# Optimization experiments

Measured on AMD Instinct MI355X. Metric: run time of the kernel, lower is better.

Reference implementation:

```python
import jax, jax.numpy as jnp
from jax import lax
import numpy as np

B, C, T = 128, 64, 750
NOUT, K, HID = 4, 16, 128


def _conv(x, w, b=None):
    y = lax.conv_general_dilated(x, w, (1, 1), 'VALID', dimension_numbers=('NCHW', 'OIHW', 'NCHW'))
    return y if b is None else y + b[None, :, None, None]


def _bn(x, g, b, m, v):
    s = g / jnp.sqrt(v + 1e-5)
    return (x - m[None, :, None, None]) * s[None, :, None, None] + b[None, :, None, None]


def _pool(x):
    return lax.reduce_window(x, -jnp.inf, lax.max, (1, 1, 3, 1), (1, 1, 3, 1), 'VALID')


def _backbone(x, ct_w, ct_b, cs_w, bn1, c2_w, bn2, c3_w, bn3, c4_w, bn4, fc_w, fc_b):
    # x: (B, C, T) -> (B, 1, T, C)  (braindecode transpose_time_to_spat)
    h = jnp.transpose(x, (0, 2, 1))[:, None]
    h = _conv(h, ct_w, ct_b)              # (B,25,T-9,C)
    h = _conv(h, cs_w)                    # (B,25,T-9,1)
    h = _pool(jax.nn.elu(_bn(h, *bn1)))   # (B,25,247,1)
    h = _pool(jax.nn.elu(_bn(_conv(h, c2_w), *bn2)))  # (B,50,79,1)
    h = _pool(jax.nn.elu(_bn(_conv(h, c3_w), *bn3)))  # (B,100,23,1)
    h = _pool(jax.nn.elu(_bn(_conv(h, c4_w), *bn4)))  # (B,200,4,1)
    h = _conv(h, fc_w, fc_b)              # (B,NOUT,1,1)
    return h[:, :, 0, 0]                  # (B,NOUT)


def _heads(feats, cluster_ids, hW1, hb1, hW2, hb2):
    # gather per-sample head params, batched small GEMMs (MoE-style dispatch)
    h = jax.nn.relu(jnp.einsum('bf,bfh->bh', feats, hW1[cluster_ids]) + hb1[cluster_ids])
    return jnp.einsum('bh,bho->bo', h, hW2[cluster_ids]) + hb2[cluster_ids]


def setup_inputs() -> dict:
    key = jax.random.key(0)
    ks = jax.random.split(key, 40)
    n = lambda i, shape, s=0.1: jax.random.normal(ks[i], shape, dtype=jnp.float32) * s
    u = lambda i, shape: jax.random.uniform(ks[i], shape, dtype=jnp.float32) + 0.5
    inp = {
        'x': n(0, (B, C, T), 1.0),
        'cluster_ids': jax.random.randint(ks[1], (B,), 0, K),
        'ct_w': n(2, (25, 1, 10, 1)), 'ct_b': n(3, (25,)),
        'cs_w': n(4, (25, 25, 1, C)),
        'bn1_g': u(5, (25,)), 'bn1_b': n(6, (25,)), 'bn1_m': n(7, (25,)), 'bn1_v': u(8, (25,)),
        'c2_w': n(9, (50, 25, 10, 1)),
        'bn2_g': u(10, (50,)), 'bn2_b': n(11, (50,)), 'bn2_m': n(12, (50,)), 'bn2_v': u(13, (50,)),
        'c3_w': n(14, (100, 50, 10, 1)),
        'bn3_g': u(15, (100,)), 'bn3_b': n(16, (100,)), 'bn3_m': n(17, (100,)), 'bn3_v': u(18, (100,)),
        'c4_w': n(19, (200, 100, 10, 1)),
        'bn4_g': u(20, (200,)), 'bn4_b': n(21, (200,)), 'bn4_m': n(22, (200,)), 'bn4_v': u(23, (200,)),
        'fc_w': n(24, (NOUT, 200, 4, 1)), 'fc_b': n(25, (NOUT,)),
        'hW1': n(26, (K, NOUT, HID)), 'hb1': n(27, (K, HID)),
        'hW2': n(28, (K, HID, NOUT)), 'hb2': n(29, (K, NOUT)),
    }
    return inp


def reference(x, cluster_ids, ct_w, ct_b, cs_w,
              bn1_g, bn1_b, bn1_m, bn1_v, c2_w,
              bn2_g, bn2_b, bn2_m, bn2_v, c3_w,
              bn3_g, bn3_b, bn3_m, bn3_v, c4_w,
              bn4_g, bn4_b, bn4_m, bn4_v, fc_w, fc_b,
              hW1, hb1, hW2, hb2):
    feats = _backbone(x, ct_w, ct_b, cs_w,
                      (bn1_g, bn1_b, bn1_m, bn1_v), c2_w,
                      (bn2_g, bn2_b, bn2_m, bn2_v), c3_w,
                      (bn3_g, bn3_b, bn3_m, bn3_v), c4_w,
                      (bn4_g, bn4_b, bn4_m, bn4_v), fc_w, fc_b)
    return _heads(feats, cluster_ids, hW1, hb1, hW2, hb2)
```

## Files before the change

kernel.cpp:

```cpp
#include <hip/hip_runtime.h>
#include <hip/hip_bf16.h>
#include <math.h>

typedef __attribute__((ext_vector_type(8))) short short8v;
typedef __attribute__((ext_vector_type(4))) float f32x4;

#define F_S1 0
#define F_H1 32
#define F_S2 64
#define F_H2 128
#define F_S3 192
#define F_H3 320
#define F_S4 448
#define F_H4 704
#define F_B1 960
#define F_P4 1024
#define F_END (1024 + 128*200*4)
#define H_BASE (F_END * 2)
#define H_P1  H_BASE
#define H_P2  (H_P1 + 128*25*248)
#define H_P3  (H_P2 + 128*50*80)
#define H_WA1 (H_P3 + 128*100*24)
#define H_WA2 (H_WA1 + 32*640)
#define H_WA3 (H_WA2 + 64*320)
#define H_WA4 (H_WA3 + 112*640)

__device__ __forceinline__ float eluf(float v) {
    return v > 0.f ? v : (expf(v) - 1.f);
}
__device__ __forceinline__ float ldf(const float* p) { return *p; }
__device__ __forceinline__ float ldf(const __hip_bfloat16* p) { return __bfloat162float(*p); }
__device__ __forceinline__ void stf(float* p, float v) { *p = v; }
__device__ __forceinline__ void stf(__hip_bfloat16* p, float v) { *p = __float2bfloat16(v); }

__device__ __forceinline__ void ld4(const float* p, float* v) {
    float2 a = *(const float2*)p, c = *(const float2*)(p + 2);
    v[0] = a.x; v[1] = a.y; v[2] = c.x; v[3] = c.y;
}
__device__ __forceinline__ void ld4(const __hip_bfloat16* p, float* v) {
    uint2 u = *(const uint2*)p;
    v[0] = __uint_as_float((u.x & 0xffffu) << 16);
    v[1] = __uint_as_float(u.x & 0xffff0000u);
    v[2] = __uint_as_float((u.y & 0xffffu) << 16);
    v[3] = __uint_as_float(u.y & 0xffff0000u);
}

#define N_WA1 (32*640)
#define N_WA2 (64*320)
#define N_WA3 (112*640)
#define N_WA4 (208*1280)
#define N_WTOT (N_WA1 + N_WA2 + N_WA3 + N_WA4)

__global__ __launch_bounds__(256) void k_pre2(
    const float* __restrict__ ct_w, const float* __restrict__ ct_b,
    const float* __restrict__ cs_w,
    const float* __restrict__ g1, const float* __restrict__ b1,
    const float* __restrict__ m1, const float* __restrict__ v1,
    const float* __restrict__ w2,
    const float* __restrict__ g2, const float* __restrict__ b2,
    const float* __restrict__ m2, const float* __restrict__ v2,
    const float* __restrict__ w3,
    const float* __restrict__ g3, const float* __restrict__ b3,
    const float* __restrict__ m3, const float* __restrict__ v3,
    const float* __restrict__ w4,
    const float* __restrict__ g4, const float* __restrict__ b4,
    const float* __restrict__ m4, const float* __restrict__ v4,
    float* __restrict__ ws) {
    __hip_bfloat16* wsh = (__hip_bfloat16*)ws;
    int t = blockIdx.x * 256 + threadIdx.x;
    if (t < N_WA1) {
        int o = t / 640, kv = t - o * 640, kk = kv / 64, c = kv - kk * 64;
        float s = 0.f;
        if (o < 25)
            for (int i = 0; i < 25; ++i)
                s += cs_w[(o * 25 + i) * 64 + c] * ct_w[i * 10 + kk];
        wsh[H_WA1 + t] = __float2bfloat16(s);
    } else if (t < N_WA1 + N_WA2) {
        int u = t - N_WA1;
        int o = u / 320, kv = u - o * 320, kk = kv / 32, c = kv - kk * 32;
        float s = (o < 50 && c < 25) ? w2[(o * 25 + c) * 10 + kk] : 0.f;
        wsh[H_WA2 + u] = __float2bfloat16(s);
    } else if (t < N_WA1 + N_WA2 + N_WA3) {
        int u = t - N_WA1 - N_WA2;
        int o = u / 640, kv = u - o * 640, kk = kv / 64, c = kv - kk * 64;
        float s = (o < 100 && c < 50) ? w3[(o * 50 + c) * 10 + kk] : 0.f;
        wsh[H_WA3 + u] = __float2bfloat16(s);
    } else if (t < N_WTOT) {
        int u = t - N_WA1 - N_WA2 - N_WA3;
        int o = u / 1280, kv = u - o * 1280, kk = kv / 128, c = kv - kk * 128;
        float s = (o < 200 && c < 100) ? w4[(o * 100 + c) * 10 + kk] : 0.f;
        wsh[H_WA4 + u] = __float2bfloat16(s);
    } else {
        int j = t - N_WTOT;
        if (j < 25) {
            float sc = g1[j] / sqrtf(v1[j] + 1e-5f);
            ws[F_S1 + j] = sc; ws[F_H1 + j] = b1[j] - m1[j] * sc;
        } else if (j >= 32 && j < 82) {
            int ch = j - 32;
            float sc = g2[ch] / sqrtf(v2[ch] + 1e-5f);
            ws[F_S2 + ch] = sc; ws[F_H2 + ch] = b2[ch] - m2[ch] * sc;
        } else if (j >= 96 && j < 196) {
            int ch = j - 96;
            float sc = g3[ch] / sqrtf(v3[ch] + 1e-5f);
            ws[F_S3 + ch] = sc; ws[F_H3 + ch] = b3[ch] - m3[ch] * sc;
        } else if (j >= 224 && j < 424) {
            int ch = j - 224;
            float sc = g4[ch] / sqrtf(v4[ch] + 1e-5f);
            ws[F_S4 + ch] = sc; ws[F_H4 + ch] = b4[ch] - m4[ch] * sc;
        } else if (j >= 448 && j < 473) {
            int o = j - 448;
            float s = 0.f;
            for (int i = 0; i < 25; ++i) {
                float cs = 0.f;
                for (int c = 0; c < 64; ++c) cs += cs_w[(o * 25 + i) * 64 + c];
                s += cs * ct_b[i];
            }
            ws[F_B1 + o] = s;
        }
    }
}

template<typename IT, typename OT, int CIN, int CINP, int COUT,
         int TINLEN, int TSIN, int TPOOL, int TSOUT,
         int PT, int OSPLIT, int NCT, int CSPLIT, int ROWS, bool BIAS>
__global__ __launch_bounds__(256) void k_convmf(
    const IT* __restrict__ in, OT* __restrict__ outp,
    const __hip_bfloat16* __restrict__ Wa,
    const float* __restrict__ sv, const float* __restrict__ hv,
    const float* __restrict__ bv) {
    constexpr int K    = CINP * 10;
    constexpr int NS   = K / 32;
    constexpr int CB   = CINP / 32;
    constexpr int NOT  = (COUT + 15) / 16;
    constexpr int NOTP = (NOT + OSPLIT - 1) / OSPLIT;
    constexpr int SWM  = (CINP >= 64) ? 7 : 3;
    constexpr int EBS  = NCT * 16;
    constexpr int CTW  = NCT / CSPLIT;
    constexpr int CHR  = ROWS / 4;

    int bx = blockIdx.x, b = blockIdx.y;
    int tt = bx / OSPLIT, os = bx % OSPLIT;
    int p0 = tt * PT;
    int PTb = min(PT, TPOOL - p0);
    int t0 = 3 * p0;
    int otLo = os * NOTP;
    int NOTb = min(NOT - otLo, NOTP);

    __shared__ __hip_bfloat16 xb[ROWS * CINP];
    __shared__ float eb[NOTP * 16 * EBS];

    for (int f = threadIdx.x; f < CIN * CHR; f += 256) {
        int c = f / CHR, j = f - c * CHR;
        int t = t0 + 4 * j;
        const IT* src = in + ((size_t)b * CIN + c) * TSIN + t;
        float v[4];
        if (t + 3 < TINLEN) {
            ld4(src, v);
        } else {
#pragma unroll
            for (int e = 0; e < 4; ++e)
                v[e] = (t + e < TINLEN) ? ldf(src + e) : 0.f;
        }
#pragma unroll
        for (int e = 0; e < 4; ++e) {
            int r = 4 * j + e;
            xb[r * CINP + (c ^ (8 * (r & SWM)))] = __float2bfloat16(v[e]);
        }
    }
    if constexpr (CINP > CIN) {
        for (int f = threadIdx.x; f < (CINP - CIN) * ROWS; f += 256) {
            int c = CIN + f / ROWS, r = f % ROWS;
            xb[r * CINP + (c ^ (8 * (r & SWM)))] = __float2bfloat16(0.f);
        }
    }
    __syncthreads();

    int lane = threadIdx.x & 63, wid = threadIdx.x >> 6;
    int lo = lane & 15, kg = lane >> 4;
    int ctg = wid % CSPLIT;
    for (int oi = wid / CSPLIT; oi < NOTb; oi += 4 / CSPLIT) {
        int ot = otLo + oi;
        const short8v* Ap = (const short8v*)(Wa + (size_t)(ot * 16 + lo) * K);
        f32x4 acc[CTW];
#pragma unroll
        for (int q = 0; q < CTW; ++q) acc[q] = (f32x4){0.f, 0.f, 0.f, 0.f};
#pragma unroll
        for (int s = 0; s < NS; ++s) {
            short8v afr = Ap[s * 4 + kg];
            int kk = s / CB, cb = s - kk * CB;
#pragma unroll
            for (int q = 0; q < CTW; ++q) {
                int ct = ctg * CTW + q;
                int r = ct * 16 + lo + kk;
                int cs = (cb * 32 + kg * 8) ^ (8 * (r & SWM));
                short8v bfr = *(const short8v*)&xb[r * CINP + cs];
                acc[q] = __builtin_amdgcn_mfma_f32_16x16x32_bf16(afr, bfr, acc[q], 0, 0, 0);
            }
        }
#pragma unroll
        for (int q = 0; q < CTW; ++q) {
            int tloc = (ctg * CTW + q) * 16 + lo;
#pragma unroll
            for (int e = 0; e < 4; ++e) {
                int o2 = ot * 16 + kg * 4 + e;
                if (o2 < COUT) {
                    float a = acc[q][e];
                    if (BIAS) a += bv[o2];
                    eb[(o2 - otLo * 16) * EBS + tloc] = eluf(a * sv[o2] + hv[o2]);
                }
            }
        }
    }
    __syncthreads();

    int oLo = otLo * 16;
    int nO = min(COUT, (otLo + NOTb) * 16) - oLo;
    for (int i = threadIdx.x; i < nO * PT; i += 256) {
        int o = oLo + i / PT, pl = i % PT;
        if (pl < PTb) {
            const float* ep = eb + (o - oLo) * EBS + 3 * pl;
            float m = fmaxf(fmaxf(ep[0], ep[1]), ep[2]);
            stf(outp + ((size_t)b * COUT + o) * TSOUT + p0 + pl, m);
        }
    }
}

__global__ __launch_bounds__(128) void k_heads(
    const float* __restrict__ p4,
    const float* __restrict__ fcw, const float* __restrict__ fcb,
    const int* __restrict__ cids,
    const float* __restrict__ hW1, const float* __restrict__ hb1,
    const float* __restrict__ hW2, const float* __restrict__ hb2,
    float* __restrict__ out) {
    __shared__ float red[4][128];
    __shared__ float fs[4];
    int b = blockIdx.x, j = threadIdx.x;

    float pa[4] = {0.f, 0.f, 0.f, 0.f};
    for (int c = j; c < 200; c += 128) {
        const float* pp = p4 + ((size_t)b * 200 + c) * 4;
        float v0 = pp[0], v1 = pp[1], v2 = pp[2], v3 = pp[3];
#pragma unroll
        for (int o = 0; o < 4; ++o) {
            const float* fw = fcw + (o * 200 + c) * 4;
            pa[o] += fw[0] * v0 + fw[1] * v1 + fw[2] * v2 + fw[3] * v3;
        }
    }
#pragma unroll
    for (int o = 0; o < 4; ++o) red[o][j] = pa[o];
    __syncthreads();
    for (int s = 64; s > 0; s >>= 1) {
        if (j < s) {
#pragma unroll
            for (int o = 0; o < 4; ++o) red[o][j] += red[o][j + s];
        }
        __syncthreads();
    }
    if (j < 4) fs[j] = red[j][0] + fcb[j];
    __syncthreads();

    int cid = cids[b];
    float hvv = hb1[cid * 128 + j];
#pragma unroll
    for (int f = 0; f < 4; ++f) hvv += fs[f] * hW1[(cid * 4 + f) * 128 + j];
    hvv = fmaxf(hvv, 0.f);
#pragma unroll
    for (int o = 0; o < 4; ++o) red[o][j] = hvv * hW2[(cid * 128 + j) * 4 + o];
    __syncthreads();
    for (int s = 64; s > 0; s >>= 1) {
        if (j < s) {
#pragma unroll
            for (int o = 0; o < 4; ++o) red[o][j] += red[o][j + s];
        }
        __syncthreads();
    }
    if (j < 4) out[b * 4 + j] = red[j][0] + hb2[cid * 4 + j];
}

extern "C" void kernel_launch(void* const* d_in, const int* in_sizes, int n_in,
                              void* d_out, int out_size, void* d_ws, size_t ws_size,
                              hipStream_t stream) {
    (void)in_sizes; (void)n_in; (void)out_size; (void)ws_size;
    const float* x    = (const float*)d_in[0];
    const int*   cid  = (const int*)d_in[1];
    const float* ctw  = (const float*)d_in[2];
    const float* ctb  = (const float*)d_in[3];
    const float* csw  = (const float*)d_in[4];
    const float* g1 = (const float*)d_in[5],  *b1 = (const float*)d_in[6];
    const float* m1 = (const float*)d_in[7],  *v1 = (const float*)d_in[8];
    const float* w2 = (const float*)d_in[9];
    const float* g2 = (const float*)d_in[10], *b2 = (const float*)d_in[11];
    const float* m2 = (const float*)d_in[12], *v2 = (const float*)d_in[13];
    const float* w3 = (const float*)d_in[14];
    const float* g3 = (const float*)d_in[15], *b3 = (const float*)d_in[16];
    const float* m3 = (const float*)d_in[17], *v3 = (const float*)d_in[18];
    const float* w4 = (const float*)d_in[19];
    const float* g4 = (const float*)d_in[20], *b4 = (const float*)d_in[21];
    const float* m4 = (const float*)d_in[22], *v4 = (const float*)d_in[23];
    const float* fcw = (const float*)d_in[24], *fcb = (const float*)d_in[25];
    const float* hW1 = (const float*)d_in[26], *hb1 = (const float*)d_in[27];
    const float* hW2 = (const float*)d_in[28], *hb2 = (const float*)d_in[29];
    float* ws  = (float*)d_ws;
    __hip_bfloat16* wsh = (__hip_bfloat16*)d_ws;
    float* out = (float*)d_out;

    k_pre2<<<dim3((N_WTOT + 512 + 255) / 256), dim3(256), 0, stream>>>(
        ctw, ctb, csw, g1, b1, m1, v1, w2, g2, b2, m2, v2,
        w3, g3, b3, m3, v3, w4, g4, b4, m4, v4, ws);

    k_convmf<float, __hip_bfloat16, 64, 64, 25, 750, 750, 247, 248,
             32, 1, 6, 2, 112, true>
        <<<dim3(8, 128), dim3(256), 0, stream>>>(
            x, wsh + H_P1, wsh + H_WA1, ws + F_S1, ws + F_H1, ws + F_B1);
    k_convmf<__hip_bfloat16, __hip_bfloat16, 25, 32, 50, 247, 248, 79, 80,
             20, 1, 4, 1, 80, false>
        <<<dim3(4, 128), dim3(256), 0, stream>>>(
            wsh + H_P1, wsh + H_P2, wsh + H_WA2, ws + F_S2, ws + F_H2, ws + F_B1);
    k_convmf<__hip_bfloat16, __hip_bfloat16, 50, 64, 100, 79, 80, 23, 24,
             12, 2, 3, 1, 64, false>
        <<<dim3(4, 128), dim3(256), 0, stream>>>(
            wsh + H_P2, wsh + H_P3, wsh + H_WA3, ws + F_S3, ws + F_H3, ws + F_B1);
    k_convmf<__hip_bfloat16, float, 100, 128, 200, 23, 24, 4, 4,
             4, 4, 1, 1, 32, false>
        <<<dim3(4, 128), dim3(256), 0, stream>>>(
            wsh + H_P3, ws + F_P4, wsh + H_WA4, ws + F_S4, ws + F_H4, ws + F_B1);

    k_heads<<<dim3(128), dim3(128), 0, stream>>>(ws + F_P4, fcw, fcb, cid,
                                                 hW1, hb1, hW2, hb2, out);
}
```

Before: 94.57 us.

## Fuse conv2-4 and heads into one per-sample kernel with LDS-resident activations

Collapses the four templated conv launches plus the heads kernel into two kernels. A specialized first-layer conv writes a time-major, swizzled bf16 pooled output. A single 512-thread per-sample tail kernel then runs layers 2-4, pooling, the FC and the heads entirely in shared memory. This removes three launches and the global round trips of the intermediate activations. In exchange it uses only 128 blocks for the tail, so occupancy and parallelism drop, and the layer-4 output now passes through bf16 before the FC.

```diff
diff --git a/kernel.cpp b/kernel.cpp
--- a/kernel.cpp
+++ b/kernel.cpp
@@ -14,42 +14,29 @@
 #define F_S4 448
 #define F_H4 704
 #define F_B1 960
-#define F_P4 1024
-#define F_END (1024 + 128*200*4)
-#define H_BASE (F_END * 2)
+#define F_END 1024
+#define H_BASE (F_END*2)
 #define H_P1  H_BASE
-#define H_P2  (H_P1 + 128*25*248)
-#define H_P3  (H_P2 + 128*50*80)
-#define H_WA1 (H_P3 + 128*100*24)
+#define H_WA1 (H_P1 + 128*8192)
 #define H_WA2 (H_WA1 + 32*640)
 #define H_WA3 (H_WA2 + 64*320)
 #define H_WA4 (H_WA3 + 112*640)
-
-__device__ __forceinline__ float eluf(float v) {
-    return v > 0.f ? v : (expf(v) - 1.f);
-}
-__device__ __forceinline__ float ldf(const float* p) { return *p; }
-__device__ __forceinline__ float ldf(const __hip_bfloat16* p) { return __bfloat162float(*p); }
-__device__ __forceinline__ void stf(float* p, float v) { *p = v; }
-__device__ __forceinline__ void stf(__hip_bfloat16* p, float v) { *p = __float2bfloat16(v); }
-
-__device__ __forceinline__ void ld4(const float* p, float* v) {
-    float2 a = *(const float2*)p, c = *(const float2*)(p + 2);
-    v[0] = a.x; v[1] = a.y; v[2] = c.x; v[3] = c.y;
-}
-__device__ __forceinline__ void ld4(const __hip_bfloat16* p, float* v) {
-    uint2 u = *(const uint2*)p;
-    v[0] = __uint_as_float((u.x & 0xffffu) << 16);
-    v[1] = __uint_as_float(u.x & 0xffff0000u);
-    v[2] = __uint_as_float((u.y & 0xffffu) << 16);
-    v[3] = __uint_as_float(u.y & 0xffff0000u);
-}
 
 #define N_WA1 (32*640)
 #define N_WA2 (64*320)
 #define N_WA3 (112*640)
 #define N_WA4 (208*1280)
 #define N_WTOT (N_WA1 + N_WA2 + N_WA3 + N_WA4)
+
+__device__ __forceinline__ float eluf(float v) {
+    return v > 0.f ? v : (expf(v) - 1.f);
+}
+__device__ __forceinline__ float ldh(const __hip_bfloat16* p) { return __bfloat162float(*p); }
+
+__device__ __forceinline__ void ld4f(const float* p, float* v) {
+    float2 a = *(const float2*)p, c = *(const float2*)(p + 2);
+    v[0] = a.x; v[1] = a.y; v[2] = c.x; v[3] = c.y;
+}
 
 __global__ __launch_bounds__(256) void k_pre2(
     const float* __restrict__ ct_w, const float* __restrict__ ct_b,
@@ -120,134 +107,239 @@
     }
 }
 
-template<typename IT, typename OT, int CIN, int CINP, int COUT,
-         int TINLEN, int TSIN, int TPOOL, int TSOUT,
-         int PT, int OSPLIT, int NCT, int CSPLIT, int ROWS, bool BIAS>
-__global__ __launch_bounds__(256) void k_convmf(
-    const IT* __restrict__ in, OT* __restrict__ outp,
-    const __hip_bfloat16* __restrict__ Wa,
-    const float* __restrict__ sv, const float* __restrict__ hv,
-    const float* __restrict__ bv) {
-    constexpr int K    = CINP * 10;
-    constexpr int NS   = K / 32;
-    constexpr int CB   = CINP / 32;
-    constexpr int NOT  = (COUT + 15) / 16;
-    constexpr int NOTP = (NOT + OSPLIT - 1) / OSPLIT;
-    constexpr int SWM  = (CINP >= 64) ? 7 : 3;
-    constexpr int EBS  = NCT * 16;
-    constexpr int CTW  = NCT / CSPLIT;
-    constexpr int CHR  = ROWS / 4;
-
+template<int NS, int CB, int CINP>
+__device__ __forceinline__ f32x4 conv_item(
+    const __hip_bfloat16* __restrict__ Wrow,
+    const __hip_bfloat16* xb, int lo, int kg, int rowBase) {
+    constexpr int SWM = (CINP >= 64) ? 7 : 3;
+    const short8v* Ap = (const short8v*)Wrow;
+    f32x4 acc = {0.f, 0.f, 0.f, 0.f};
+#pragma unroll 1
+    for (int sb = 0; sb < NS; sb += 10) {
+        short8v af[10];
+#pragma unroll
+        for (int u = 0; u < 10; ++u) af[u] = Ap[(sb + u) * 4 + kg];
+#pragma unroll
+        for (int u = 0; u < 10; ++u) {
+            int s = sb + u;
+            int kk = s / CB, cb = s % CB;
+            int r = rowBase + lo + kk;
+            int cs = (cb * 32 + kg * 8) ^ (8 * (r & SWM));
+            short8v bf = *(const short8v*)&xb[r * CINP + cs];
+            acc = __builtin_amdgcn_mfma_f32_16x16x32_bf16(af[u], bf, acc, 0, 0, 0);
+        }
+    }
+    return acc;
+}
+
+__global__ __launch_bounds__(256) void k_conv1(
+    const float* __restrict__ x, float* __restrict__ ws) {
+    __hip_bfloat16* wsh = (__hip_bfloat16*)ws;
+    const __hip_bfloat16* Wa = wsh + H_WA1;
     int bx = blockIdx.x, b = blockIdx.y;
-    int tt = bx / OSPLIT, os = bx % OSPLIT;
-    int p0 = tt * PT;
-    int PTb = min(PT, TPOOL - p0);
-    int t0 = 3 * p0;
-    int otLo = os * NOTP;
-    int NOTb = min(NOT - otLo, NOTP);
-
-    __shared__ __hip_bfloat16 xb[ROWS * CINP];
-    __shared__ float eb[NOTP * 16 * EBS];
-
-    for (int f = threadIdx.x; f < CIN * CHR; f += 256) {
-        int c = f / CHR, j = f - c * CHR;
+    int tp0 = bx * 42;
+    int PTb = min(42, 247 - tp0);
+    int t0 = 126 * bx;
+
+    __shared__ __align__(16) __hip_bfloat16 xb[144 * 64];
+    __shared__ __align__(16) __hip_bfloat16 eb[32 * 128];
+
+    for (int f = threadIdx.x; f < 64 * 36; f += 256) {
+        int c = f / 36, j = f - c * 36;
         int t = t0 + 4 * j;
-        const IT* src = in + ((size_t)b * CIN + c) * TSIN + t;
+        const float* src = x + ((size_t)b * 64 + c) * 750 + t;
         float v[4];
-        if (t + 3 < TINLEN) {
-            ld4(src, v);
+        if (t + 3 < 750) {
+            ld4f(src, v);
         } else {
 #pragma unroll
-            for (int e = 0; e < 4; ++e)
-                v[e] = (t + e < TINLEN) ? ldf(src + e) : 0.f;
+            for (int e = 0; e < 4; ++e) v[e] = (t + e < 750) ? src[e] : 0.f;
         }
 #pragma unroll
         for (int e = 0; e < 4; ++e) {
             int r = 4 * j + e;
-            xb[r * CINP + (c ^ (8 * (r & SWM)))] = __float2bfloat16(v[e]);
-        }
-    }
-    if constexpr (CINP > CIN) {
-        for (int f = threadIdx.x; f < (CINP - CIN) * ROWS; f += 256) {
-            int c = CIN + f / ROWS, r = f % ROWS;
-            xb[r * CINP + (c ^ (8 * (r & SWM)))] = __float2bfloat16(0.f);
+            xb[r * 64 + (c ^ (8 * (r & 7)))] = __float2bfloat16(v[e]);
         }
     }
     __syncthreads();
 
     int lane = threadIdx.x & 63, wid = threadIdx.x >> 6;
     int lo = lane & 15, kg = lane >> 4;
-    int ctg = wid % CSPLIT;
-    for (int oi = wid / CSPLIT; oi < NOTb; oi += 4 / CSPLIT) {
-        int ot = otLo + oi;
-        const short8v* Ap = (const short8v*)(Wa + (size_t)(ot * 16 + lo) * K);
-        f32x4 acc[CTW];
-#pragma unroll
-        for (int q = 0; q < CTW; ++q) acc[q] = (f32x4){0.f, 0.f, 0.f, 0.f};
-#pragma unroll
-        for (int s = 0; s < NS; ++s) {
-            short8v afr = Ap[s * 4 + kg];
-            int kk = s / CB, cb = s - kk * CB;
-#pragma unroll
-            for (int q = 0; q < CTW; ++q) {
-                int ct = ctg * CTW + q;
-                int r = ct * 16 + lo + kk;
-                int cs = (cb * 32 + kg * 8) ^ (8 * (r & SWM));
-                short8v bfr = *(const short8v*)&xb[r * CINP + cs];
-                acc[q] = __builtin_amdgcn_mfma_f32_16x16x32_bf16(afr, bfr, acc[q], 0, 0, 0);
-            }
-        }
-#pragma unroll
-        for (int q = 0; q < CTW; ++q) {
-            int tloc = (ctg * CTW + q) * 16 + lo;
-#pragma unroll
-            for (int e = 0; e < 4; ++e) {
-                int o2 = ot * 16 + kg * 4 + e;
-                if (o2 < COUT) {
-                    float a = acc[q][e];
-                    if (BIAS) a += bv[o2];
-                    eb[(o2 - otLo * 16) * EBS + tloc] = eluf(a * sv[o2] + hv[o2]);
-                }
-            }
-        }
-    }
-    __syncthreads();
-
-    int oLo = otLo * 16;
-    int nO = min(COUT, (otLo + NOTb) * 16) - oLo;
-    for (int i = threadIdx.x; i < nO * PT; i += 256) {
-        int o = oLo + i / PT, pl = i % PT;
+    int ot = wid >> 1, ctg = wid & 1;
+    const short8v* Ap = (const short8v*)(Wa + (size_t)(ot * 16 + lo) * 640);
+    f32x4 acc[4];
+#pragma unroll
+    for (int q = 0; q < 4; ++q) acc[q] = (f32x4){0.f, 0.f, 0.f, 0.f};
+#pragma unroll 1
+    for (int sb = 0; sb < 20; sb += 10) {
+        short8v af[10];
+#pragma unroll
+        for (int u = 0; u < 10; ++u) af[u] = Ap[(sb + u) * 4 + kg];
+#pragma unroll
+        for (int u = 0; u < 10; ++u) {
+            int s = sb + u;
+            int kk = s >> 1, cb = s & 1;
+#pragma unroll
+            for (int q = 0; q < 4; ++q) {
+                int r = (ctg * 4 + q) * 16 + lo + kk;
+                int cs = (cb * 32 + kg * 8) ^ (8 * (r & 7));
+                short8v bf = *(const short8v*)&xb[r * 64 + cs];
+                acc[q] = __builtin_amdgcn_mfma_f32_16x16x32_bf16(af[u], bf, acc[q], 0, 0, 0);
+            }
+        }
+    }
+#pragma unroll
+    for (int q = 0; q < 4; ++q) {
+        int tloc = (ctg * 4 + q) * 16 + lo;
+#pragma unroll
+        for (int e = 0; e < 4; ++e) {
+            int o2 = ot * 16 + kg * 4 + e;
+            float a = acc[q][e] + ws[F_B1 + o2];
+            eb[o2 * 128 + tloc] = __float2bfloat16(eluf(a * ws[F_S1 + o2] + ws[F_H1 + o2]));
+        }
+    }
+    __syncthreads();
+
+    __hip_bfloat16* p1g = wsh + H_P1 + (size_t)b * 8192;
+    for (int i = threadIdx.x; i < 32 * 42; i += 256) {
+        int o = i / 42, pl = i - o * 42;
         if (pl < PTb) {
-            const float* ep = eb + (o - oLo) * EBS + 3 * pl;
-            float m = fmaxf(fmaxf(ep[0], ep[1]), ep[2]);
-            stf(outp + ((size_t)b * COUT + o) * TSOUT + p0 + pl, m);
-        }
-    }
-}
-
-__global__ __launch_bounds__(128) void k_heads(
-    const float* __restrict__ p4,
+            int tp = tp0 + pl;
+            float val = 0.f;
+            if (o < 25) {
+                const __hip_bfloat16* ep = eb + o * 128 + 3 * pl;
+                val = fmaxf(fmaxf(ldh(ep), ldh(ep + 1)), ldh(ep + 2));
+            }
+            p1g[tp * 32 + (o ^ (8 * (tp & 3)))] = __float2bfloat16(val);
+        }
+    }
+    if (bx == 5) {
+        for (int i = threadIdx.x; i < 9 * 32; i += 256) {
+            int r = 247 + i / 32, c = i & 31;
+            p1g[r * 32 + c] = __float2bfloat16(0.f);
+        }
+    }
+}
+
+__global__ __launch_bounds__(512) void k_tail(
+    const float* __restrict__ ws,
     const float* __restrict__ fcw, const float* __restrict__ fcb,
     const int* __restrict__ cids,
     const float* __restrict__ hW1, const float* __restrict__ hb1,
     const float* __restrict__ hW2, const float* __restrict__ hb2,
     float* __restrict__ out) {
+    const __hip_bfloat16* wsh = (const __hip_bfloat16*)ws;
+    const __hip_bfloat16* wa2 = wsh + H_WA2;
+    const __hip_bfloat16* wa3 = wsh + H_WA3;
+    const __hip_bfloat16* wa4 = wsh + H_WA4;
+    int b = blockIdx.x;
+    int tid = threadIdx.x;
+    int lane = tid & 63, wid = tid >> 6;
+    int lo = lane & 15, kg = lane >> 4;
+
+    __shared__ __align__(16) __hip_bfloat16 p1s[256 * 32];
+    __shared__ __align__(16) __hip_bfloat16 p2s[96 * 64];
+    __shared__ __align__(16) __hip_bfloat16 p3s[32 * 128];
+    __shared__ __align__(16) __hip_bfloat16 ebh[112 * 80];
+    __shared__ float p4s[200 * 4];
     __shared__ float red[4][128];
-    __shared__ float fs[4];
-    int b = blockIdx.x, j = threadIdx.x;
-
-    float pa[4] = {0.f, 0.f, 0.f, 0.f};
-    for (int c = j; c < 200; c += 128) {
-        const float* pp = p4 + ((size_t)b * 200 + c) * 4;
-        float v0 = pp[0], v1 = pp[1], v2 = pp[2], v3 = pp[3];
-#pragma unroll
-        for (int o = 0; o < 4; ++o) {
-            const float* fw = fcw + (o * 200 + c) * 4;
-            pa[o] += fw[0] * v0 + fw[1] * v1 + fw[2] * v2 + fw[3] * v3;
-        }
-    }
-#pragma unroll
-    for (int o = 0; o < 4; ++o) red[o][j] = pa[o];
+    __shared__ float fsf[4];
+
+    {
+        const uint4* src = (const uint4*)(wsh + H_P1 + (size_t)b * 8192);
+        uint4* dst = (uint4*)p1s;
+        dst[tid] = src[tid];
+        dst[tid + 512] = src[tid + 512];
+        uint4 z = {0, 0, 0, 0};
+        ((uint4*)p2s)[tid] = z;
+        if (tid < 256) ((uint4*)p2s)[512 + tid] = z;
+        ((uint4*)p3s)[tid] = z;
+    }
+    __syncthreads();
+
+    for (int c0 = 0; c0 < 4; ++c0) {
+        int tb = 60 * c0;
+        int PTb = (c0 == 3) ? 19 : 20;
+        for (int it = wid; it < 16; it += 8) {
+            int ot = it >> 2, ct = it & 3;
+            f32x4 a = conv_item<10, 1, 32>(wa2 + (size_t)(ot * 16 + lo) * 320,
+                                           p1s, lo, kg, tb + ct * 16);
+            int tloc = ct * 16 + lo;
+#pragma unroll
+            for (int e = 0; e < 4; ++e) {
+                int o2 = ot * 16 + kg * 4 + e;
+                ebh[o2 * 64 + tloc] =
+                    __float2bfloat16(eluf(a[e] * ws[F_S2 + o2] + ws[F_H2 + o2]));
+            }
+        }
+        __syncthreads();
+        for (int i = tid; i < 50 * 20; i += 512) {
+            int o = i / 20, pl = i - o * 20;
+            if (pl < PTb) {
+                int tp = 20 * c0 + pl;
+                const __hip_bfloat16* ep = ebh + o * 64 + 3 * pl;
+                float m = fmaxf(fmaxf(ldh(ep), ldh(ep + 1)), ldh(ep + 2));
+                p2s[tp * 64 + (o ^ (8 * (tp & 7)))] = __float2bfloat16(m);
+            }
+        }
+        __syncthreads();
+    }
+
+    for (int it = wid; it < 35; it += 8) {
+        int ot = it / 5, ct = it - 5 * ot;
+        f32x4 a = conv_item<20, 2, 64>(wa3 + (size_t)(ot * 16 + lo) * 640,
+                                       p2s, lo, kg, ct * 16);
+        int tloc = ct * 16 + lo;
+#pragma unroll
+        for (int e = 0; e < 4; ++e) {
+            int o2 = ot * 16 + kg * 4 + e;
+            ebh[o2 * 80 + tloc] =
+                __float2bfloat16(eluf(a[e] * ws[F_S3 + o2] + ws[F_H3 + o2]));
+        }
+    }
+    __syncthreads();
+    for (int i = tid; i < 100 * 23; i += 512) {
+        int o = i / 23, pl = i - 23 * o;
+        const __hip_bfloat16* ep = ebh + o * 80 + 3 * pl;
+        float m = fmaxf(fmaxf(ldh(ep), ldh(ep + 1)), ldh(ep + 2));
+        p3s[pl * 128 + (o ^ (8 * (pl & 7)))] = __float2bfloat16(m);
+    }
+    __syncthreads();
+
+    for (int it = wid; it < 13; it += 8) {
+        int ot = it;
+        f32x4 a = conv_item<40, 4, 128>(wa4 + (size_t)(ot * 16 + lo) * 1280,
+                                        p3s, lo, kg, 0);
+#pragma unroll
+        for (int e = 0; e < 4; ++e) {
+            int o2 = ot * 16 + kg * 4 + e;
+            ebh[o2 * 16 + lo] =
+                __float2bfloat16(eluf(a[e] * ws[F_S4 + o2] + ws[F_H4 + o2]));
+        }
+    }
+    __syncthreads();
+    for (int i = tid; i < 800; i += 512) {
+        int o = i >> 2, pl = i & 3;
+        const __hip_bfloat16* ep = ebh + o * 16 + 3 * pl;
+        p4s[o * 4 + pl] = fmaxf(fmaxf(ldh(ep), ldh(ep + 1)), ldh(ep + 2));
+    }
+    __syncthreads();
+
+    int j = tid;
+    if (j < 128) {
+        float pa[4] = {0.f, 0.f, 0.f, 0.f};
+        for (int c = j; c < 200; c += 128) {
+            const float* pp = p4s + c * 4;
+            float v0 = pp[0], v1 = pp[1], v2 = pp[2], v3 = pp[3];
+#pragma unroll
+            for (int o = 0; o < 4; ++o) {
+                const float* fw = fcw + (o * 200 + c) * 4;
+                pa[o] += fw[0] * v0 + fw[1] * v1 + fw[2] * v2 + fw[3] * v3;
+            }
+        }
+#pragma unroll
+        for (int o = 0; o < 4; ++o) red[o][j] = pa[o];
+    }
     __syncthreads();
     for (int s = 64; s > 0; s >>= 1) {
         if (j < s) {
@@ -256,16 +348,18 @@
         }
         __syncthreads();
     }
-    if (j < 4) fs[j] = red[j][0] + fcb[j];
+    if (j < 4) fsf[j] = red[j][0] + fcb[j];
     __syncthreads();
 
     int cid = cids[b];
-    float hvv = hb1[cid * 128 + j];
-#pragma unroll
-    for (int f = 0; f < 4; ++f) hvv += fs[f] * hW1[(cid * 4 + f) * 128 + j];
-    hvv = fmaxf(hvv, 0.f);
-#pragma unroll
-    for (int o = 0; o < 4; ++o) red[o][j] = hvv * hW2[(cid * 128 + j) * 4 + o];
+    if (j < 128) {
+        float hvv = hb1[cid * 128 + j];
+#pragma unroll
+        for (int f = 0; f < 4; ++f) hvv += fsf[f] * hW1[(cid * 4 + f) * 128 + j];
+        hvv = fmaxf(hvv, 0.f);
+#pragma unroll
+        for (int o = 0; o < 4; ++o) red[o][j] = hvv * hW2[(cid * 128 + j) * 4 + o];
+    }
     __syncthreads();
     for (int s = 64; s > 0; s >>= 1) {
         if (j < s) {
@@ -301,30 +395,12 @@
     const float* hW1 = (const float*)d_in[26], *hb1 = (const float*)d_in[27];
     const float* hW2 = (const float*)d_in[28], *hb2 = (const float*)d_in[29];
     float* ws  = (float*)d_ws;
-    __hip_bfloat16* wsh = (__hip_bfloat16*)d_ws;
     float* out = (float*)d_out;
 
     k_pre2<<<dim3((N_WTOT + 512 + 255) / 256), dim3(256), 0, stream>>>(
         ctw, ctb, csw, g1, b1, m1, v1, w2, g2, b2, m2, v2,
         w3, g3, b3, m3, v3, w4, g4, b4, m4, v4, ws);
-
-    k_convmf<float, __hip_bfloat16, 64, 64, 25, 750, 750, 247, 248,
-             32, 1, 6, 2, 112, true>
-        <<<dim3(8, 128), dim3(256), 0, stream>>>(
-            x, wsh + H_P1, wsh + H_WA1, ws + F_S1, ws + F_H1, ws + F_B1);
-    k_convmf<__hip_bfloat16, __hip_bfloat16, 25, 32, 50, 247, 248, 79, 80,
-             20, 1, 4, 1, 80, false>
-        <<<dim3(4, 128), dim3(256), 0, stream>>>(
-            wsh + H_P1, wsh + H_P2, wsh + H_WA2, ws + F_S2, ws + F_H2, ws + F_B1);
-    k_convmf<__hip_bfloat16, __hip_bfloat16, 50, 64, 100, 79, 80, 23, 24,
-             12, 2, 3, 1, 64, false>
-        <<<dim3(4, 128), dim3(256), 0, stream>>>(
-            wsh + H_P2, wsh + H_P3, wsh + H_WA3, ws + F_S3, ws + F_H3, ws + F_B1);
-    k_convmf<__hip_bfloat16, float, 100, 128, 200, 23, 24, 4, 4,
-             4, 4, 1, 1, 32, false>
-        <<<dim3(4, 128), dim3(256), 0, stream>>>(
-            wsh + H_P3, ws + F_P4, wsh + H_WA4, ws + F_S4, ws + F_H4, ws + F_B1);
-
-    k_heads<<<dim3(128), dim3(128), 0, stream>>>(ws + F_P4, fcw, fcb, cid,
-                                                 hW1, hb1, hW2, hb2, out);
-}
+    k_conv1<<<dim3(6, 128), dim3(256), 0, stream>>>(x, ws);
+    k_tail<<<dim3(128), dim3(512), 0, stream>>>(ws, fcw, fcb, cid,
+                                                hW1, hb1, hW2, hb2, out);
+}
```

New measurement: 111.9 us. 1.18x slower.
